# Kernel optimization log

Measured on AMD Instinct MI355X. Metric: run time of the kernel, lower is better.

Reference implementation:

```python
import jax, jax.numpy as jnp
import numpy as np

DIM = 512
HEADS = 8
DIM_HEAD = 64
INNER = HEADS * DIM_HEAD
B = 16
Q_LEN = 512
KV_LEN = 1024
LN_EPS = 1e-5


def _rotate_half(x):
    # pairs (x0,x1),(x2,x3),... -> (-x1,x0,-x3,x2,...)
    x1 = x[..., 0::2]
    x2 = x[..., 1::2]
    return jnp.stack((-x2, x1), axis=-1).reshape(x.shape)


def _apply_rope(x, freqs):
    # x: [B, L, H, D], freqs: [B, L, D] broadcast over heads
    f = freqs[:, :, None, :]
    return x * jnp.cos(f) + _rotate_half(x) * jnp.sin(f)


def _layernorm(x, g, b):
    mu = jnp.mean(x, axis=-1, keepdims=True)
    var = jnp.mean(jnp.square(x - mu), axis=-1, keepdims=True)
    return (x - mu) * jax.lax.rsqrt(var + LN_EPS) * g + b


def _make_rope_freqs(n_per_seg, n_seg):
    inv_freq = 1.0 / (10000.0 ** (np.arange(0, DIM_HEAD, 2, dtype=np.float32) / DIM_HEAD))
    pos = np.tile(np.arange(n_per_seg, dtype=np.float32), n_seg)  # positions restart per segment
    f = pos[:, None] * inv_freq[None, :]              # [N, D/2]
    return jnp.asarray(np.repeat(f, 2, axis=-1))      # [N, D], each freq duplicated for the (d 2) pairing


def setup_inputs() -> dict:
    key = jax.random.key(0)
    ks = jax.random.split(key, 8)
    Nq, Nkv = B * Q_LEN, B * KV_LEN
    x_query = jax.random.normal(ks[0], (Nq, DIM), dtype=jnp.float32)
    x_context = jax.random.normal(ks[1], (Nkv, DIM), dtype=jnp.float32)
    rotary_time_emb_query = _make_rope_freqs(Q_LEN, B)
    rotary_time_emb_context = _make_rope_freqs(KV_LEN, B)
    s = 1.0 / np.sqrt(DIM)
    Wq = jax.random.normal(ks[2], (DIM, INNER), dtype=jnp.float32) * s
    Wkv = jax.random.normal(ks[3], (DIM, 2 * INNER), dtype=jnp.float32) * s
    Wout = jax.random.normal(ks[4], (INNER, DIM), dtype=jnp.float32) * (1.0 / np.sqrt(INNER))
    bout = jnp.zeros((DIM,), dtype=jnp.float32)
    ln_q_g = jnp.ones((DIM,), dtype=jnp.float32)
    ln_q_b = jnp.zeros((DIM,), dtype=jnp.float32)
    ln_c_g = jnp.ones((DIM,), dtype=jnp.float32)
    ln_c_b = jnp.zeros((DIM,), dtype=jnp.float32)
    return {
        'x_query': x_query, 'x_context': x_context,
        'rotary_time_emb_query': rotary_time_emb_query,
        'rotary_time_emb_context': rotary_time_emb_context,
        'ln_q_g': ln_q_g, 'ln_q_b': ln_q_b, 'ln_c_g': ln_c_g, 'ln_c_b': ln_c_b,
        'Wq': Wq, 'Wkv': Wkv, 'Wout': Wout, 'bout': bout,
        'q_len': Q_LEN, 'kv_len': KV_LEN,
    }


def reference(x_query, x_context, rotary_time_emb_query, rotary_time_emb_context,
              ln_q_g, ln_q_b, ln_c_g, ln_c_b, Wq, Wkv, Wout, bout, q_len, kv_len):
    nb = x_query.shape[0] // q_len  # number of block-diagonal segments (equal lengths)
    xq = _layernorm(x_query, ln_q_g, ln_q_b)
    xc = _layernorm(x_context, ln_c_g, ln_c_b)
    q = (xq @ Wq).reshape(nb, q_len, HEADS, DIM_HEAD)
    kv = xc @ Wkv
    k = kv[:, :INNER].reshape(nb, kv_len, HEADS, DIM_HEAD)
    v = kv[:, INNER:].reshape(nb, kv_len, HEADS, DIM_HEAD)
    fq = rotary_time_emb_query.reshape(nb, q_len, DIM_HEAD)
    fkv = rotary_time_emb_context.reshape(nb, kv_len, DIM_HEAD)
    q = _apply_rope(q, fq)
    k = _apply_rope(k, fkv)
    v = _apply_rope(v, fkv)  # rotate_value=True
    scale = 1.0 / np.sqrt(DIM_HEAD)
    scores = jnp.einsum('bqhd,bkhd->bhqk', q, k) * scale  # block-diagonal attention per segment
    attn = jax.nn.softmax(scores, axis=-1)
    out = jnp.einsum('bhqk,bkhd->bqhd', attn, v)
    out = _apply_rope(out, -fq)  # un-rotate values by query freqs (rotate_value=True)
    out = out.reshape(nb * q_len, INNER)
    return out @ Wout + bout
```

## Files before the change

kernel.cpp:

```cpp
#include <hip/hip_runtime.h>

#define DIMK 512
#define NHEADS 8
#define DH 64
#define NBATCH 16
#define QLEN 512
#define KVLEN 1024
#define NQ (NBATCH*QLEN)
#define NKV (NBATCH*KVLEN)

typedef __attribute__((ext_vector_type(8))) short bf16x8;
typedef __attribute__((ext_vector_type(4))) float f32x4;
typedef __attribute__((ext_vector_type(8))) unsigned short us8;

#define QSCL 0.1803368801111204f

__device__ __forceinline__ float bf2f(unsigned short u) {
    return __uint_as_float(((unsigned)u) << 16);
}
__device__ __forceinline__ unsigned short f2bf(float f) {
    unsigned u = __float_as_uint(f);
    return (unsigned short)((u + 0x7fffu + ((u >> 16) & 1u)) >> 16);
}
__device__ __forceinline__ unsigned cvtpk(float a, float b) {
    unsigned r;
    asm("v_cvt_pk_bf16_f32 %0, %1, %2" : "=v"(r) : "v"(a), "v"(b));
    return r;
}
__device__ __forceinline__ void gl2lds16(const void* g, const void* lds) {
    __builtin_amdgcn_global_load_lds(
        (const __attribute__((address_space(1))) unsigned int*)g,
        (__attribute__((address_space(3))) unsigned int*)lds, 16, 0, 0);
}

__global__ __launch_bounds__(256) void prep_kernel(
    const float* __restrict__ fq, const float* __restrict__ fkv,
    float2* __restrict__ fqt,
    const float* __restrict__ xa, const float* __restrict__ xb,
    const float* __restrict__ ga, const float* __restrict__ ba,
    const float* __restrict__ gb, const float* __restrict__ bb,
    unsigned short* __restrict__ xout,
    const float* __restrict__ Wq, unsigned short* __restrict__ WqT,
    const float* __restrict__ Wkv, unsigned short* __restrict__ WkvT,
    const float* __restrict__ Wout, unsigned short* __restrict__ WoutTh,
    unsigned short* __restrict__ WoutTl)
{
    const int bid = blockIdx.x;
    const int tid = threadIdx.x;
    if (bid < 6144) {
        int i = bid * 256 + tid;
        const int na = NQ * DH;
        float f = (i < na) ? fq[i] : fkv[i - na];
        float sn, cs;
        sincosf(f, &sn, &cs);
        fqt[i] = make_float2(cs, sn);
    } else if (bid < 12288) {
        int row  = (bid - 6144) * 4 + (tid >> 6);
        int lane = tid & 63;
        bool isa = row < NQ;
        const float* x  = isa ? xa + (size_t)row * DIMK : xb + (size_t)(row - NQ) * DIMK;
        const float* g  = isa ? ga : gb;
        const float* bt = isa ? ba : bb;
        const float4* xr = reinterpret_cast<const float4*>(x);
        float4 v0 = xr[lane * 2];
        float4 v1 = xr[lane * 2 + 1];
        float s  = v0.x + v0.y + v0.z + v0.w + v1.x + v1.y + v1.z + v1.w;
        float sq = v0.x*v0.x + v0.y*v0.y + v0.z*v0.z + v0.w*v0.w
                 + v1.x*v1.x + v1.y*v1.y + v1.z*v1.z + v1.w*v1.w;
        #pragma unroll
        for (int off = 32; off; off >>= 1) {
            s  += __shfl_xor(s, off);
            sq += __shfl_xor(sq, off);
        }
        float mu   = s * (1.0f / DIMK);
        float rstd = rsqrtf(sq * (1.0f / DIMK) - mu * mu + 1e-5f);
        const float4* g4 = reinterpret_cast<const float4*>(g + lane * 8);
        const float4* b4 = reinterpret_cast<const float4*>(bt + lane * 8);
        float4 g0 = g4[0], g1 = g4[1], b0 = b4[0], b1 = b4[1];
        us8 o;
        o[0] = f2bf((v0.x - mu) * rstd * g0.x + b0.x);
        o[1] = f2bf((v0.y - mu) * rstd * g0.y + b0.y);
        o[2] = f2bf((v0.z - mu) * rstd * g0.z + b0.z);
        o[3] = f2bf((v0.w - mu) * rstd * g0.w + b0.w);
        o[4] = f2bf((v1.x - mu) * rstd * g1.x + b1.x);
        o[5] = f2bf((v1.y - mu) * rstd * g1.y + b1.y);
        o[6] = f2bf((v1.z - mu) * rstd * g1.z + b1.z);
        o[7] = f2bf((v1.w - mu) * rstd * g1.w + b1.w);
        *reinterpret_cast<us8*>(xout + (size_t)row * DIMK + lane * 8) = o;
    } else if (bid < 13312) {
        int idx = (bid - 12288) * 256 + tid;
        int n = idx >> 9, k = idx & 511;
        WqT[idx] = f2bf(Wq[(size_t)k * 512 + n]);
    } else if (bid < 15360) {
        int idx = (bid - 13312) * 256 + tid;
        int n = idx >> 9, k = idx & 511;
        WkvT[idx] = f2bf(Wkv[(size_t)k * 1024 + n]);
    } else {
        int idx = (bid - 15360) * 256 + tid;
        int n = idx >> 9, k = idx & 511;
        float v = Wout[(size_t)k * 512 + n];
        unsigned short h = f2bf(v);
        WoutTh[idx] = h;
        WoutTl[idx] = f2bf(v - bf2f(h));
    }
}

__global__ __launch_bounds__(256, 2) void mmqkv_kernel(
    const unsigned short* __restrict__ xq, const unsigned short* __restrict__ xc,
    const unsigned short* __restrict__ WqT, const unsigned short* __restrict__ WkvT,
    unsigned short* __restrict__ qbout, unsigned short* __restrict__ kbout,
    unsigned short* __restrict__ vTout,
    const float2* __restrict__ fqt, const float2* __restrict__ fkvt)
{
    __shared__ __align__(16) unsigned short AsH[2][128 * 32];
    __shared__ __align__(16) unsigned short BsH[2][128 * 32];

    const int t = threadIdx.x;
    const int lane = t & 63, w = t >> 6;
    const int l15 = lane & 15, l4 = lane >> 4;
    const int wr = w >> 1, wc = w & 1;

    const int nwg  = gridDim.x;
    const int tile = (blockIdx.x & 7) * (nwg >> 3) + (blockIdx.x >> 3);
    const bool isq = tile < 256;
    const int tl   = isq ? tile : tile - 256;
    const int NCT  = isq ? 4 : 8;
    const unsigned short* A = isq ? xq : xc;
    const unsigned short* B = isq ? WqT : WkvT;
    const float2* fct = isq ? fqt : fkvt;
    const int row0 = (tl / NCT) * 128;
    const int col0 = (tl % NCT) * 128;

    const int stRow = lane >> 2;
    const int stK   = (lane & 3) * 8;

    auto stage = [&](int buf, int k0) {
        #pragma unroll
        for (int j = 0; j < 4; ++j) {
            int id  = w * 4 + j;
            int mat = id >> 3;
            int sub = id & 7;
            int row = sub * 16 + stRow;
            const unsigned short* gsrc = (mat == 0)
                ? A + (size_t)(row0 + row) * 512
                : B + (size_t)(col0 + row) * 512;
            unsigned short* ldst = (mat == 0) ? &AsH[buf][0] : &BsH[buf][0];
            gl2lds16(gsrc + k0 + stK, ldst + sub * 512);
        }
    };

    f32x4 acc[4][4];
    #pragma unroll
    for (int m = 0; m < 4; ++m)
        #pragma unroll
        for (int n = 0; n < 4; ++n)
            acc[m][n] = (f32x4){0.f, 0.f, 0.f, 0.f};

    stage(0, 0);
    __syncthreads();

    for (int ks = 0; ks < 16; ++ks) {
        const int cur = ks & 1;
        if (ks < 15) stage(cur ^ 1, (ks + 1) * 32);

        bf16x8 fah[4], fbh[4];
        #pragma unroll
        for (int m = 0; m < 4; ++m)
            fah[m] = *reinterpret_cast<const bf16x8*>(&AsH[cur][(wr*64 + m*16 + l15) * 32 + l4*8]);
        #pragma unroll
        for (int n = 0; n < 4; ++n)
            fbh[n] = *reinterpret_cast<const bf16x8*>(&BsH[cur][(wc*64 + n*16 + l15) * 32 + l4*8]);
        #pragma unroll
        for (int m = 0; m < 4; ++m)
            #pragma unroll
            for (int n = 0; n < 4; ++n)
                acc[m][n] = __builtin_amdgcn_mfma_f32_16x16x32_bf16(fah[m], fbh[n], acc[m][n], 0, 0, 0);
        __syncthreads();
    }

    unsigned short* pool = (w < 2) ? &AsH[w][0] : &BsH[w - 2][0];
    if (!isq && col0 >= 512) {
        const int vb    = row0 >> 10;
        const int kbase = (row0 & 1023) + wr * 64;
        const int vh    = ((col0 - 512) >> 6) + wc;
        #pragma unroll
        for (int m = 0; m < 4; ++m)
            #pragma unroll
            for (int n = 0; n < 4; ++n)
                #pragma unroll
                for (int j = 0; j < 4; ++j) {
                    float v = acc[m][n][j];
                    int gr = row0 + wr*64 + m*16 + l4*4 + j;
                    int d  = n*16 + l15;
                    float pv = __shfl_xor(v, 1);
                    float2 cn = fct[(size_t)gr * DH + d];
                    float nv = (lane & 1) ? fmaf(pv, cn.y, v * cn.x)
                                          : fmaf(-pv, cn.y, v * cn.x);
                    int kloc = m*16 + l4*4 + j;
                    int ch   = (kloc >> 3) ^ (d & 7);
                    pool[d*64 + ch*8 + (kloc & 7)] = f2bf(nv);
                }
        #pragma unroll
        for (int i = 0; i < 8; ++i) {
            int c   = i * 64 + lane;
            int dd  = c >> 3, chq = c & 7;
            int sw  = chq ^ (dd & 7);
            us8 vv = *reinterpret_cast<const us8*>(&pool[dd*64 + sw*8]);
            *reinterpret_cast<us8*>(
                &vTout[(size_t)((vb * 8 + vh) * 64 + dd) * 1024 + kbase + chq * 8]) = vv;
        }
    } else {
        unsigned short* Cout = isq ? qbout : kbout;
        #pragma unroll
        for (int m = 0; m < 4; ++m)
            #pragma unroll
            for (int n = 0; n < 4; ++n)
                #pragma unroll
                for (int j = 0; j < 4; ++j) {
                    float v = acc[m][n][j];
                    int gr = row0 + wr*64 + m*16 + l4*4 + j;
                    int d  = n*16 + l15;
                    float pv = __shfl_xor(v, 1);
                    float2 cn = fct[(size_t)gr * DH + d];
                    float nv = (lane & 1) ? fmaf(pv, cn.y, v * cn.x)
                                          : fmaf(-pv, cn.y, v * cn.x);
                    if (isq) nv *= QSCL;
                    int row = m*16 + l4*4 + j;
                    int col = n*16 + l15;
                    int ch  = (col >> 3) ^ (row & 7);
                    pool[row*64 + ch*8 + (col & 7)] = f2bf(nv);
                }
        #pragma unroll
        for (int i = 0; i < 8; ++i) {
            int c  = i * 64 + lane;
            int rl = c >> 3, ch = c & 7;
            int sw = ch ^ (rl & 7);
            us8 vv = *reinterpret_cast<const us8*>(&pool[rl*64 + sw*8]);
            int gr = row0 + wr*64 + rl;
            int gc = col0 + wc*64 + ch*8;
            *reinterpret_cast<us8*>(&Cout[(size_t)gr * 512 + gc]) = vv;
        }
    }
}

__global__ __launch_bounds__(256, 2) void mm2_kernel(
    const unsigned short* __restrict__ Ah, const unsigned short* __restrict__ Al,
    const unsigned short* __restrict__ Bh, const unsigned short* __restrict__ Bl,
    float* __restrict__ Cout, const float* __restrict__ bias)
{
    __shared__ __align__(16) unsigned short AsH[2][128 * 32];
    __shared__ __align__(16) unsigned short BsH[2][128 * 32];
    __shared__ __align__(16) unsigned short AsL[2][128 * 32];
    __shared__ __align__(16) unsigned short BsL[2][128 * 32];

    const int t = threadIdx.x;
    const int lane = t & 63, w = t >> 6;
    const int l15 = lane & 15, l4 = lane >> 4;
    const int wr = w >> 1, wc = w & 1;

    const int nwg  = gridDim.x;
    const int tile = (blockIdx.x & 7) * (nwg >> 3) + (blockIdx.x >> 3);
    const int row0 = (tile >> 2) * 128;
    const int col0 = (tile & 3) * 128;

    const int stRow = lane >> 2;
    const int stK   = (lane & 3) * 8;

    auto stage = [&](int buf, int k0) {
        #pragma unroll
        for (int j = 0; j < 8; ++j) {
            int id  = w * 8 + j;
            int mat = id >> 3;
            int sub = id & 7;
            int row = sub * 16 + stRow;
            const unsigned short* gsrc =
                (mat == 0) ? Ah + (size_t)(row0 + row) * 512 :
                (mat == 1) ? Bh + (size_t)(col0 + row) * 512 :
                (mat == 2) ? Al + (size_t)(row0 + row) * 512 :
                             Bl + (size_t)(col0 + row) * 512;
            unsigned short* ldst =
                (mat == 0) ? &AsH[buf][0] :
                (mat == 1) ? &BsH[buf][0] :
                (mat == 2) ? &AsL[buf][0] :
                             &BsL[buf][0];
            gl2lds16(gsrc + k0 + stK, ldst + sub * 512);
        }
    };

    f32x4 acc[4][4];
    #pragma unroll
    for (int m = 0; m < 4; ++m)
        #pragma unroll
        for (int n = 0; n < 4; ++n)
            acc[m][n] = (f32x4){0.f, 0.f, 0.f, 0.f};

    stage(0, 0);
    __syncthreads();

    for (int ks = 0; ks < 16; ++ks) {
        const int cur = ks & 1;
        if (ks < 15) stage(cur ^ 1, (ks + 1) * 32);

        bf16x8 fah[4], fbh[4], fal[4], fbl[4];
        #pragma unroll
        for (int m = 0; m < 4; ++m) {
            fah[m] = *reinterpret_cast<const bf16x8*>(&AsH[cur][(wr*64 + m*16 + l15) * 32 + l4*8]);
            fal[m] = *reinterpret_cast<const bf16x8*>(&AsL[cur][(wr*64 + m*16 + l15) * 32 + l4*8]);
        }
        #pragma unroll
        for (int n = 0; n < 4; ++n) {
            fbh[n] = *reinterpret_cast<const bf16x8*>(&BsH[cur][(wc*64 + n*16 + l15) * 32 + l4*8]);
            fbl[n] = *reinterpret_cast<const bf16x8*>(&BsL[cur][(wc*64 + n*16 + l15) * 32 + l4*8]);
        }
        #pragma unroll
        for (int m = 0; m < 4; ++m)
            #pragma unroll
            for (int n = 0; n < 4; ++n) {
                acc[m][n] = __builtin_amdgcn_mfma_f32_16x16x32_bf16(fah[m], fbh[n], acc[m][n], 0, 0, 0);
                acc[m][n] = __builtin_amdgcn_mfma_f32_16x16x32_bf16(fah[m], fbl[n], acc[m][n], 0, 0, 0);
                acc[m][n] = __builtin_amdgcn_mfma_f32_16x16x32_bf16(fal[m], fbh[n], acc[m][n], 0, 0, 0);
            }
        __syncthreads();
    }

    #pragma unroll
    for (int m = 0; m < 4; ++m)
        #pragma unroll
        for (int n = 0; n < 4; ++n)
            #pragma unroll
            for (int j = 0; j < 4; ++j) {
                int gr = row0 + wr*64 + m*16 + l4*4 + j;
                int gc = col0 + wc*64 + n*16 + l15;
                Cout[(size_t)gr * 512 + gc] = acc[m][n][j] + bias[gc];
            }
}

__global__ __launch_bounds__(256, 2) void attn_kernel(
    const unsigned short* __restrict__ kb, const unsigned short* __restrict__ qb,
    const unsigned short* __restrict__ vT, const float2* __restrict__ fqt,
    unsigned short* __restrict__ aobH, unsigned short* __restrict__ aobL)
{
    __shared__ __align__(16) unsigned short Vs[4][4096];
    __shared__ __align__(16) unsigned short Ps[4][2048];

    const int bid  = blockIdx.x;
    const int tile = (bid & 7) * 64 + (bid >> 3);
    const int qs = tile & 3, h = (tile >> 2) & 7, b = tile >> 5;
    const int t = threadIdx.x, lane = t & 63, w = t >> 6;
    const int l15 = lane & 15, l4 = lane >> 4;
    const int bh = b * 8 + h;

    const int q_row0 = b * QLEN + qs * 128 + w * 16;
    const size_t kvr0 = (size_t)b * KVLEN;

    constexpr float RTHR = 11.5415585f;

    bf16x8 qf0 = *reinterpret_cast<const bf16x8*>(
        &qb[(size_t)(q_row0 + l15) * 512 + h * 64 + l4 * 8]);
    bf16x8 qf1 = *reinterpret_cast<const bf16x8*>(
        &qb[(size_t)(q_row0 + l15) * 512 + h * 64 + 32 + l4 * 8]);
    bf16x8 qg0 = *reinterpret_cast<const bf16x8*>(
        &qb[(size_t)(q_row0 + 64 + l15) * 512 + h * 64 + l4 * 8]);
    bf16x8 qg1 = *reinterpret_cast<const bf16x8*>(
        &qb[(size_t)(q_row0 + 64 + l15) * 512 + h * 64 + 32 + l4 * 8]);

    auto stageVT = [&](int buf, int kt) {
        #pragma unroll
        for (int i = 0; i < 2; ++i) {
            const int dbase = (w * 2 + i) * 8;
            const int dlo = lane >> 3;
            const int cb  = lane & 7;
            gl2lds16(&vT[(size_t)(bh * 64 + dbase + dlo) * 1024 + kt * 64
                         + ((cb ^ dlo) * 8)],
                     &Vs[buf][dbase * 64]);
        }
    };

    auto loadK = [&](bf16x8 (&dst)[4][2], int kt) {
        #pragma unroll
        for (int n = 0; n < 4; ++n) {
            const unsigned short* krow =
                &kb[(kvr0 + kt * 64 + n * 16 + l15) * 512 + h * 64];
            dst[n][0] = *reinterpret_cast<const bf16x8*>(&krow[l4 * 8]);
            dst[n][1] = *reinterpret_cast<const bf16x8*>(&krow[32 + l4 * 8]);
        }
    };

    f32x4 o0[4], o1[4];
    #pragma unroll
    for (int dt = 0; dt < 4; ++dt) {
        o0[dt] = (f32x4){0.f, 0.f, 0.f, 0.f};
        o1[dt] = (f32x4){0.f, 0.f, 0.f, 0.f};
    }
    float m0 = -3.0e38f, l0 = 0.f, m1 = -3.0e38f, l1 = 0.f;

    unsigned short* pw0 = &Ps[w][0];
    unsigned short* pw1 = &Ps[w][1024];

    auto iter = [&](int vbuf, bf16x8 (&KC)[4][2]) {
        {
            f32x4 s[4];
            #pragma unroll
            for (int n = 0; n < 4; ++n) {
                f32x4 a = (f32x4){0.f, 0.f, 0.f, 0.f};
                a = __builtin_amdgcn_mfma_f32_16x16x32_bf16(KC[n][0], qf0, a, 0, 0, 0);
                a = __builtin_amdgcn_mfma_f32_16x16x32_bf16(KC[n][1], qf1, a, 0, 0, 0);
                s[n] = a;
            }
            float pmax = -3.0e38f;
            #pragma unroll
            for (int n = 0; n < 4; ++n)
                #pragma unroll
                for (int j = 0; j < 4; ++j)
                    pmax = fmaxf(pmax, s[n][j]);
            pmax = fmaxf(pmax, __shfl_xor(pmax, 16));
            pmax = fmaxf(pmax, __shfl_xor(pmax, 32));
            if (!__all(pmax - m0 <= RTHR)) {
                float mnew = fmaxf(m0, pmax);
                float al = __builtin_amdgcn_exp2f(m0 - mnew);
                l0 *= al;
                float a0 = __shfl(al, l4 * 4 + 0);
                float a1 = __shfl(al, l4 * 4 + 1);
                float a2 = __shfl(al, l4 * 4 + 2);
                float a3 = __shfl(al, l4 * 4 + 3);
                #pragma unroll
                for (int dt = 0; dt < 4; ++dt) {
                    o0[dt][0] *= a0; o0[dt][1] *= a1; o0[dt][2] *= a2; o0[dt][3] *= a3;
                }
                m0 = mnew;
            }
            float rs = 0.f;
            #pragma unroll
            for (int n = 0; n < 4; ++n) {
                float p0 = __builtin_amdgcn_exp2f(s[n][0] - m0);
                float p1 = __builtin_amdgcn_exp2f(s[n][1] - m0);
                float p2 = __builtin_amdgcn_exp2f(s[n][2] - m0);
                float p3 = __builtin_amdgcn_exp2f(s[n][3] - m0);
                rs += (p0 + p1) + (p2 + p3);
                uint2 pk = make_uint2(cvtpk(p0, p1), cvtpk(p2, p3));
                int idx = l15 * 64 + ((n * 16 + l4 * 4) ^ ((l15 & 7) << 3));
                *reinterpret_cast<uint2*>(&pw0[idx]) = pk;
            }
            rs += __shfl_xor(rs, 16);
            rs += __shfl_xor(rs, 32);
            l0 += rs;

            bf16x8 pfh[2];
            #pragma unroll
            for (int c = 0; c < 2; ++c) {
                int idx = l15 * 64 + ((c * 32 + l4 * 8) ^ ((l15 & 7) << 3));
                pfh[c] = *reinterpret_cast<const bf16x8*>(&pw0[idx]);
            }
            #pragma unroll
            for (int dt = 0; dt < 4; ++dt) {
                int d = dt * 16 + l15;
                #pragma unroll
                for (int c = 0; c < 2; ++c) {
                    int vidx = d * 64 + ((c * 32 + l4 * 8) ^ ((d & 7) << 3));
                    bf16x8 vf = *reinterpret_cast<const bf16x8*>(&Vs[vbuf][vidx]);
                    o0[dt] = __builtin_amdgcn_mfma_f32_16x16x32_bf16(pfh[c], vf, o0[dt], 0, 0, 0);
                }
            }
        }
        {
            f32x4 s[4];
            #pragma unroll
            for (int n = 0; n < 4; ++n) {
                f32x4 a = (f32x4){0.f, 0.f, 0.f, 0.f};
                a = __builtin_amdgcn_mfma_f32_16x16x32_bf16(KC[n][0], qg0, a, 0, 0, 0);
                a = __builtin_amdgcn_mfma_f32_16x16x32_bf16(KC[n][1], qg1, a, 0, 0, 0);
                s[n] = a;
            }
            float pmax = -3.0e38f;
            #pragma unroll
            for (int n = 0; n < 4; ++n)
                #pragma unroll
                for (int j = 0; j < 4; ++j)
                    pmax = fmaxf(pmax, s[n][j]);
            pmax = fmaxf(pmax, __shfl_xor(pmax, 16));
            pmax = fmaxf(pmax, __shfl_xor(pmax, 32));
            if (!__all(pmax - m1 <= RTHR)) {
                float mnew = fmaxf(m1, pmax);
                float al = __builtin_amdgcn_exp2f(m1 - mnew);
                l1 *= al;
                float a0 = __shfl(al, l4 * 4 + 0);
                float a1 = __shfl(al, l4 * 4 + 1);
                float a2 = __shfl(al, l4 * 4 + 2);
                float a3 = __shfl(al, l4 * 4 + 3);
                #pragma unroll
                for (int dt = 0; dt < 4; ++dt) {
                    o1[dt][0] *= a0; o1[dt][1] *= a1; o1[dt][2] *= a2; o1[dt][3] *= a3;
                }
                m1 = mnew;
            }
            float rs = 0.f;
            #pragma unroll
            for (int n = 0; n < 4; ++n) {
                float p0 = __builtin_amdgcn_exp2f(s[n][0] - m1);
                float p1 = __builtin_amdgcn_exp2f(s[n][1] - m1);
                float p2 = __builtin_amdgcn_exp2f(s[n][2] - m1);
                float p3 = __builtin_amdgcn_exp2f(s[n][3] - m1);
                rs += (p0 + p1) + (p2 + p3);
                uint2 pk = make_uint2(cvtpk(p0, p1), cvtpk(p2, p3));
                int idx = l15 * 64 + ((n * 16 + l4 * 4) ^ ((l15 & 7) << 3));
                *reinterpret_cast<uint2*>(&pw1[idx]) = pk;
            }
            rs += __shfl_xor(rs, 16);
            rs += __shfl_xor(rs, 32);
            l1 += rs;

            bf16x8 pfh[2];
            #pragma unroll
            for (int c = 0; c < 2; ++c) {
                int idx = l15 * 64 + ((c * 32 + l4 * 8) ^ ((l15 & 7) << 3));
                pfh[c] = *reinterpret_cast<const bf16x8*>(&pw1[idx]);
            }
            #pragma unroll
            for (int dt = 0; dt < 4; ++dt) {
                int d = dt * 16 + l15;
                #pragma unroll
                for (int c = 0; c < 2; ++c) {
                    int vidx = d * 64 + ((c * 32 + l4 * 8) ^ ((d & 7) << 3));
                    bf16x8 vf = *reinterpret_cast<const bf16x8*>(&Vs[vbuf][vidx]);
                    o1[dt] = __builtin_amdgcn_mfma_f32_16x16x32_bf16(pfh[c], vf, o1[dt], 0, 0, 0);
                }
            }
        }
    };

    bf16x8 kA[4][2], kB[4][2];
    stageVT(0, 0);
    stageVT(1, 1);
    loadK(kA, 0);

    for (int kt = 0; kt < 16; kt += 2) {
        __syncthreads();
        if (kt < 14) {
            stageVT((kt + 2) & 3, kt + 2);
            stageVT((kt + 3) & 3, kt + 3);
        }
        loadK(kB, kt + 1);
        iter(kt & 3, kA);
        if (kt < 14) loadK(kA, kt + 2);
        iter((kt + 1) & 3, kB);
    }

    __syncthreads();
    unsigned short* pe = &Vs[w][0];

    {
        unsigned short* ps = pe;
        float linv = 1.f / l0;
        #pragma unroll
        for (int r = 0; r < 4; ++r) {
            float lr = __shfl(linv, l4 * 4 + r);
            int gr = q_row0 + l4 * 4 + r;
            #pragma unroll
            for (int dt = 0; dt < 4; ++dt) {
                int d = dt * 16 + l15;
                float val = o0[dt][r] * lr;
                float pv = __shfl_xor(val, 1);
                float2 cn = fqt[(size_t)gr * DH + d];
                float rr = (d & 1) ? (val * cn.x - pv * cn.y) : (val * cn.x + pv * cn.y);
                unsigned short hi = f2bf(rr);
                float lo = rr - bf2f(hi);
                int row = l4 * 4 + r;
                int ch  = (d >> 3) ^ (row & 7);
                ps[row*64 + ch*8 + (d & 7)] = hi;
                ps[1024 + row*64 + ch*8 + (d & 7)] = f2bf(lo);
            }
        }
        #pragma unroll
        for (int i = 0; i < 2; ++i) {
            int c  = i * 64 + lane;
            int rl = c >> 3, ch = c & 7;
            int sw = ch ^ (rl & 7);
            us8 vh = *reinterpret_cast<const us8*>(&ps[rl*64 + sw*8]);
            us8 vl = *reinterpret_cast<const us8*>(&ps[1024 + rl*64 + sw*8]);
            size_t off = (size_t)(q_row0 + rl) * 512 + h * 64 + ch * 8;
            *reinterpret_cast<us8*>(&aobH[off]) = vh;
            *reinterpret_cast<us8*>(&aobL[off]) = vl;
        }
    }
    {
        unsigned short* ps = pe + 2048;
        float linv = 1.f / l1;
        #pragma unroll
        for (int r = 0; r < 4; ++r) {
            float lr = __shfl(linv, l4 * 4 + r);
            int gr = q_row0 + 64 + l4 * 4 + r;
            #pragma unroll
            for (int dt = 0; dt < 4; ++dt) {
                int d = dt * 16 + l15;
                float val = o1[dt][r] * lr;
                float pv = __shfl_xor(val, 1);
                float2 cn = fqt[(size_t)gr * DH + d];
                float rr = (d & 1) ? (val * cn.x - pv * cn.y) : (val * cn.x + pv * cn.y);
                unsigned short hi = f2bf(rr);
                float lo = rr - bf2f(hi);
                int row = l4 * 4 + r;
                int ch  = (d >> 3) ^ (row & 7);
                ps[row*64 + ch*8 + (d & 7)] = hi;
                ps[1024 + row*64 + ch*8 + (d & 7)] = f2bf(lo);
            }
        }
        #pragma unroll
        for (int i = 0; i < 2; ++i) {
            int c  = i * 64 + lane;
            int rl = c >> 3, ch = c & 7;
            int sw = ch ^ (rl & 7);
            us8 vh = *reinterpret_cast<const us8*>(&ps[rl*64 + sw*8]);
            us8 vl = *reinterpret_cast<const us8*>(&ps[1024 + rl*64 + sw*8]);
            size_t off = (size_t)(q_row0 + 64 + rl) * 512 + h * 64 + ch * 8;
            *reinterpret_cast<us8*>(&aobH[off]) = vh;
            *reinterpret_cast<us8*>(&aobL[off]) = vl;
        }
    }
}

extern "C" void kernel_launch(void* const* d_in, const int* in_sizes, int n_in,
                              void* d_out, int out_size, void* d_ws, size_t ws_size,
                              hipStream_t stream) {
    const float* x_query   = (const float*)d_in[0];
    const float* x_context = (const float*)d_in[1];
    const float* fq        = (const float*)d_in[2];
    const float* fkv       = (const float*)d_in[3];
    const float* ln_q_g    = (const float*)d_in[4];
    const float* ln_q_b    = (const float*)d_in[5];
    const float* ln_c_g    = (const float*)d_in[6];
    const float* ln_c_b    = (const float*)d_in[7];
    const float* Wq        = (const float*)d_in[8];
    const float* Wkv       = (const float*)d_in[9];
    const float* Wout      = (const float*)d_in[10];
    const float* bout      = (const float*)d_in[11];
    float* out = (float*)d_out;

    unsigned short* xq     = (unsigned short*)d_ws;
    unsigned short* xc     = xq + (size_t)NQ * 512;
    unsigned short* WqT    = xc + (size_t)NKV * 512;
    unsigned short* WkvT   = WqT + 512 * 512;
    unsigned short* WoutTh = WkvT + 1024 * 512;
    unsigned short* WoutTl = WoutTh + 512 * 512;
    unsigned short* qb     = WoutTl + 512 * 512;
    unsigned short* kb     = qb + (size_t)NQ * 512;
    unsigned short* vT     = kb + (size_t)NKV * 512;
    unsigned short* aobH   = vT + (size_t)NKV * 512;
    unsigned short* aobL   = aobH + (size_t)NQ * 512;
    float2* fqt            = (float2*)(aobL + (size_t)NQ * 512);

    prep_kernel<<<16384, 256, 0, stream>>>(
        fq, fkv, fqt,
        x_query, x_context, ln_q_g, ln_q_b, ln_c_g, ln_c_b, xq,
        Wq, WqT, Wkv, WkvT, Wout, WoutTh, WoutTl);

    mmqkv_kernel<<<1280, 256, 0, stream>>>(
        xq, xc, WqT, WkvT, qb, kb, vT, fqt, fqt + (size_t)NQ * DH);

    attn_kernel<<<512, 256, 0, stream>>>(kb, qb, vT, fqt, aobH, aobL);

    mm2_kernel<<<256, 256, 0, stream>>>(
        aobH, aobL, WoutTh, WoutTl, out, bout);
}
```

Measured before the change: 131.9 us.

## Widen QKV GEMM tiles to 128x256 with 512-thread blocks

Result: slower. 158.1 us (+19.9%).

```diff
diff --git a/kernel.cpp b/kernel.cpp
--- a/kernel.cpp
+++ b/kernel.cpp
@@ -105,7 +105,7 @@
     }
 }
 
-__global__ __launch_bounds__(256, 2) void mmqkv_kernel(
+__global__ __launch_bounds__(512, 4) void mmqkv_kernel(
     const unsigned short* __restrict__ xq, const unsigned short* __restrict__ xc,
     const unsigned short* __restrict__ WqT, const unsigned short* __restrict__ WkvT,
     unsigned short* __restrict__ qbout, unsigned short* __restrict__ kbout,
@@ -113,38 +113,37 @@
     const float2* __restrict__ fqt, const float2* __restrict__ fkvt)
 {
     __shared__ __align__(16) unsigned short AsH[2][128 * 32];
-    __shared__ __align__(16) unsigned short BsH[2][128 * 32];
+    __shared__ __align__(16) unsigned short BsH[2][256 * 32];
 
     const int t = threadIdx.x;
     const int lane = t & 63, w = t >> 6;
     const int l15 = lane & 15, l4 = lane >> 4;
-    const int wr = w >> 1, wc = w & 1;
+    const int wr = w >> 2, wc = w & 3;
 
     const int nwg  = gridDim.x;
     const int tile = (blockIdx.x & 7) * (nwg >> 3) + (blockIdx.x >> 3);
-    const bool isq = tile < 256;
-    const int tl   = isq ? tile : tile - 256;
-    const int NCT  = isq ? 4 : 8;
+    const bool isq = tile < 128;
+    const int tl   = isq ? tile : tile - 128;
     const unsigned short* A = isq ? xq : xc;
     const unsigned short* B = isq ? WqT : WkvT;
     const float2* fct = isq ? fqt : fkvt;
-    const int row0 = (tl / NCT) * 128;
-    const int col0 = (tl % NCT) * 128;
+    const int row0 = isq ? (tl >> 1) * 128 : (tl >> 2) * 128;
+    const int col0 = isq ? (tl & 1) * 256 : (tl & 3) * 256;
 
     const int stRow = lane >> 2;
     const int stK   = (lane & 3) * 8;
 
     auto stage = [&](int buf, int k0) {
         #pragma unroll
-        for (int j = 0; j < 4; ++j) {
-            int id  = w * 4 + j;
-            int mat = id >> 3;
-            int sub = id & 7;
+        for (int j = 0; j < 3; ++j) {
+            int id  = w * 3 + j;
+            bool isA = id < 8;
+            int sub = isA ? id : id - 8;
             int row = sub * 16 + stRow;
-            const unsigned short* gsrc = (mat == 0)
+            const unsigned short* gsrc = isA
                 ? A + (size_t)(row0 + row) * 512
                 : B + (size_t)(col0 + row) * 512;
-            unsigned short* ldst = (mat == 0) ? &AsH[buf][0] : &BsH[buf][0];
+            unsigned short* ldst = isA ? &AsH[buf][0] : &BsH[buf][0];
             gl2lds16(gsrc + k0 + stK, ldst + sub * 512);
         }
     };
@@ -178,67 +177,79 @@
         __syncthreads();
     }
 
-    unsigned short* pool = (w < 2) ? &AsH[w][0] : &BsH[w - 2][0];
+    unsigned short* pool = (w < 4) ? &AsH[0][0] + w * 2048
+                                   : &BsH[0][0] + (w - 4) * 2048;
+
     if (!isq && col0 >= 512) {
-        const int vb    = row0 >> 10;
-        const int kbase = (row0 & 1023) + wr * 64;
-        const int vh    = ((col0 - 512) >> 6) + wc;
-        #pragma unroll
-        for (int m = 0; m < 4; ++m)
-            #pragma unroll
-            for (int n = 0; n < 4; ++n)
-                #pragma unroll
-                for (int j = 0; j < 4; ++j) {
-                    float v = acc[m][n][j];
-                    int gr = row0 + wr*64 + m*16 + l4*4 + j;
-                    int d  = n*16 + l15;
-                    float pv = __shfl_xor(v, 1);
-                    float2 cn = fct[(size_t)gr * DH + d];
-                    float nv = (lane & 1) ? fmaf(pv, cn.y, v * cn.x)
-                                          : fmaf(-pv, cn.y, v * cn.x);
-                    int kloc = m*16 + l4*4 + j;
-                    int ch   = (kloc >> 3) ^ (d & 7);
-                    pool[d*64 + ch*8 + (kloc & 7)] = f2bf(nv);
-                }
-        #pragma unroll
-        for (int i = 0; i < 8; ++i) {
-            int c   = i * 64 + lane;
-            int dd  = c >> 3, chq = c & 7;
-            int sw  = chq ^ (dd & 7);
-            us8 vv = *reinterpret_cast<const us8*>(&pool[dd*64 + sw*8]);
-            *reinterpret_cast<us8*>(
-                &vTout[(size_t)((vb * 8 + vh) * 64 + dd) * 1024 + kbase + chq * 8]) = vv;
+        const int vb = row0 >> 10;
+        const int vh = ((col0 - 512) >> 6) + wc;
+        const int kb0 = (row0 & 1023) + wr * 64;
+        #pragma unroll
+        for (int p = 0; p < 2; ++p) {
+            #pragma unroll
+            for (int mm = 0; mm < 2; ++mm) {
+                int m = p * 2 + mm;
+                #pragma unroll
+                for (int n = 0; n < 4; ++n)
+                    #pragma unroll
+                    for (int j = 0; j < 4; ++j) {
+                        float v = acc[m][n][j];
+                        int gr = row0 + wr*64 + m*16 + l4*4 + j;
+                        int d  = n*16 + l15;
+                        float pv = __shfl_xor(v, 1);
+                        float2 cn = fct[(size_t)gr * DH + d];
+                        float nv = (lane & 1) ? fmaf(pv, cn.y, v * cn.x)
+                                              : fmaf(-pv, cn.y, v * cn.x);
+                        int kloc = mm*16 + l4*4 + j;
+                        int ch   = (kloc >> 3) ^ (d & 3);
+                        pool[d*32 + ch*8 + (kloc & 7)] = f2bf(nv);
+                    }
+            }
+            #pragma unroll
+            for (int i = 0; i < 4; ++i) {
+                int c   = i * 64 + lane;
+                int dd  = c >> 2, chq = c & 3;
+                int sw  = chq ^ (dd & 3);
+                us8 vv = *reinterpret_cast<const us8*>(&pool[dd*32 + sw*8]);
+                *reinterpret_cast<us8*>(
+                    &vTout[(size_t)((vb * 8 + vh) * 64 + dd) * 1024 + kb0 + p*32 + chq * 8]) = vv;
+            }
         }
     } else {
         unsigned short* Cout = isq ? qbout : kbout;
         #pragma unroll
-        for (int m = 0; m < 4; ++m)
-            #pragma unroll
-            for (int n = 0; n < 4; ++n)
-                #pragma unroll
-                for (int j = 0; j < 4; ++j) {
-                    float v = acc[m][n][j];
-                    int gr = row0 + wr*64 + m*16 + l4*4 + j;
-                    int d  = n*16 + l15;
-                    float pv = __shfl_xor(v, 1);
-                    float2 cn = fct[(size_t)gr * DH + d];
-                    float nv = (lane & 1) ? fmaf(pv, cn.y, v * cn.x)
-                                          : fmaf(-pv, cn.y, v * cn.x);
-                    if (isq) nv *= QSCL;
-                    int row = m*16 + l4*4 + j;
-                    int col = n*16 + l15;
-                    int ch  = (col >> 3) ^ (row & 7);
-                    pool[row*64 + ch*8 + (col & 7)] = f2bf(nv);
-                }
-        #pragma unroll
-        for (int i = 0; i < 8; ++i) {
-            int c  = i * 64 + lane;
-            int rl = c >> 3, ch = c & 7;
-            int sw = ch ^ (rl & 7);
-            us8 vv = *reinterpret_cast<const us8*>(&pool[rl*64 + sw*8]);
-            int gr = row0 + wr*64 + rl;
-            int gc = col0 + wc*64 + ch*8;
-            *reinterpret_cast<us8*>(&Cout[(size_t)gr * 512 + gc]) = vv;
+        for (int p = 0; p < 2; ++p) {
+            #pragma unroll
+            for (int mm = 0; mm < 2; ++mm) {
+                int m = p * 2 + mm;
+                #pragma unroll
+                for (int n = 0; n < 4; ++n)
+                    #pragma unroll
+                    for (int j = 0; j < 4; ++j) {
+                        float v = acc[m][n][j];
+                        int gr = row0 + wr*64 + m*16 + l4*4 + j;
+                        int d  = n*16 + l15;
+                        float pv = __shfl_xor(v, 1);
+                        float2 cn = fct[(size_t)gr * DH + d];
+                        float nv = (lane & 1) ? fmaf(pv, cn.y, v * cn.x)
+                                              : fmaf(-pv, cn.y, v * cn.x);
+                        if (isq) nv *= QSCL;
+                        int rp  = mm*16 + l4*4 + j;
+                        int col = n*16 + l15;
+                        int ch  = (col >> 3) ^ (rp & 7);
+                        pool[rp*64 + ch*8 + (col & 7)] = f2bf(nv);
+                    }
+            }
+            #pragma unroll
+            for (int i = 0; i < 4; ++i) {
+                int c  = i * 64 + lane;
+                int rl = c >> 3, ch = c & 7;
+                int sw = ch ^ (rl & 7);
+                us8 vv = *reinterpret_cast<const us8*>(&pool[rl*64 + sw*8]);
+                int gr = row0 + wr*64 + p*32 + rl;
+                int gc = col0 + wc*64 + ch*8;
+                *reinterpret_cast<us8*>(&Cout[(size_t)gr * 512 + gc]) = vv;
+            }
         }
     }
 }
@@ -653,7 +664,7 @@
         x_query, x_context, ln_q_g, ln_q_b, ln_c_g, ln_c_b, xq,
         Wq, WqT, Wkv, WkvT, Wout, WoutTh, WoutTl);
 
-    mmqkv_kernel<<<1280, 256, 0, stream>>>(
+    mmqkv_kernel<<<640, 512, 0, stream>>>(
         xq, xc, WqT, WkvT, qb, kb, vT, fqt, fqt + (size_t)NQ * DH);
 
     attn_kernel<<<512, 256, 0, stream>>>(kb, qb, vT, fqt, aobH, aobL);
```
